# Kernel tuning notes

Measured on AMD Instinct MI355X. Metric: run time of the kernel, lower is better.

## Reference

```python
import jax, jax.numpy as jnp
import numpy as np

N = 50000
E = 1600000
DIM = 128
RC = 5.0
DEPTH = 3


def setup_inputs() -> dict:
    key = jax.random.key(0)
    kv, ke, ks, kd, kw, kb, krs, ksig = jax.random.split(key, 8)
    v = jax.random.normal(kv, (N, DIM), dtype=jnp.float32)
    # edge distances in [0, rc]
    e = jax.random.uniform(ke, (E, 1), dtype=jnp.float32) * RC
    src = jax.random.randint(ks, (E,), 0, N, dtype=jnp.int32)
    dst = jax.random.randint(kd, (E,), 0, N, dtype=jnp.int32)
    # learned params: A = nn.Linear(dim, dim); rs, sigma = torch.rand(1)
    A_w = jax.random.normal(kw, (DIM, DIM), dtype=jnp.float32) / np.sqrt(DIM)
    A_b = jax.random.normal(kb, (DIM,), dtype=jnp.float32) * 0.01
    rs = jax.random.uniform(krs, (1,), dtype=jnp.float32)
    sigma = jax.random.uniform(ksig, (1,), dtype=jnp.float32)
    return {"v": v, "e": e, "src": src, "dst": dst,
            "A_w": A_w, "A_b": A_b, "rs": rs, "sigma": sigma}


def _edge_envelope(r, rs, sigma):
    # exp(-(r-rs)^2/sigma^2) * 0.5 * cos(pi*r/rc) * (r < rc)
    gauss = jnp.exp(-jnp.square(r - rs) / jnp.square(sigma))
    cutoff = 0.5 * jnp.cos(np.pi * r / RC) * (r < RC).astype(r.dtype)
    return gauss * cutoff


def reference(v, e, src, dst, A_w, A_b, rs, sigma):
    f = _edge_envelope(e, rs, sigma)  # [E, 1]
    cur = v
    for _ in range(DEPTH):
        msg = f * cur[src]  # gather src node feats, weight by edge envelope: [E, DIM]
        svf = jax.ops.segment_sum(msg, dst, num_segments=N)  # scatter-sum to dst: [N, DIM]
        cur = jax.nn.relu((svf + v) @ A_w.T + A_b)  # linear + relu, skip from original v
    return cur
```

## Files before the change

kernel.cpp:

```cpp
#include <hip/hip_runtime.h>
#include <math.h>

#define N_NODES 50000
#define N_PAD   50048
#define N_EDGES 1600000
#define DIM     128
#define RCUT    5.0f
#define NGROUP  (N_PAD / 64)
#define NB_PRE  512
#define CH_PRE  (N_EDGES / NB_PRE)
#define NB_CONV 6250
#define NB_WPREP 8
#define NB_SUB  8
#define B_SUB   (NB_PRE / NB_SUB)
#define XPAD    136
#define NTILE   (N_PAD / 16)

typedef __attribute__((ext_vector_type(8))) __bf16 bf16x8;
typedef __attribute__((ext_vector_type(4))) float  f32x4;

__device__ __forceinline__ float bf_lo(unsigned int u) { return __uint_as_float(u << 16); }
__device__ __forceinline__ float bf_hi(unsigned int u) { return __uint_as_float(u & 0xffff0000u); }
__device__ __forceinline__ unsigned short f2bf(float x) {
    unsigned int u = __float_as_uint(x);
    u += 0x7fffu + ((u >> 16) & 1u);
    return (unsigned short)(u >> 16);
}

__global__ __launch_bounds__(256) void preA_kernel(
        const float* __restrict__ v, unsigned short* __restrict__ vb,
        const float* __restrict__ Aw, uint4* __restrict__ wfrag,
        const int* __restrict__ dst, int* __restrict__ partial) {
    int b = blockIdx.x;
    if (b < NB_CONV) {
        int i = b * 256 + threadIdx.x;
        float4 x = ((const float4*)v)[i];
        uint2 o;
        o.x = (unsigned)f2bf(x.x) | ((unsigned)f2bf(x.y) << 16);
        o.y = (unsigned)f2bf(x.z) | ((unsigned)f2bf(x.w) << 16);
        ((uint2*)vb)[i] = o;
    } else if (b < NB_CONV + NB_WPREP) {
        int t = (b - NB_CONV) * 256 + threadIdx.x;
        int lane = t & 63, nt = (t >> 6) & 7, kk = t >> 9;
        int n  = nt * 16 + (lane & 15);
        int k0 = kk * 32 + (lane >> 4) * 8;
        unsigned short h[8];
        #pragma unroll
        for (int i = 0; i < 8; ++i) h[i] = f2bf(Aw[n * DIM + k0 + i]);
        uint4 o;
        o.x = h[0] | ((unsigned)h[1] << 16); o.y = h[2] | ((unsigned)h[3] << 16);
        o.z = h[4] | ((unsigned)h[5] << 16); o.w = h[6] | ((unsigned)h[7] << 16);
        wfrag[t] = o;
    } else {
        __shared__ int h[NGROUP];
        int cb = b - NB_CONV - NB_WPREP, tid = threadIdx.x;
        for (int g = tid; g < NGROUP; g += 256) h[g] = 0;
        __syncthreads();
        int beg = cb * CH_PRE, end = beg + CH_PRE;
        for (int i = beg + tid; i < end; i += 256)
            atomicAdd(&h[dst[i] >> 6], 1);
        __syncthreads();
        for (int g = tid; g < NGROUP; g += 256) partial[cb * NGROUP + g] = h[g];
    }
}

__global__ __launch_bounds__(256) void ktot2_kernel(const int* __restrict__ partial,
                                                    int* __restrict__ partial2) {
    int gb = blockIdx.x & 3, bb = blockIdx.x >> 2;
    int g = gb * 256 + threadIdx.x;
    if (g >= NGROUP) return;
    int s = 0;
    int b0 = bb * B_SUB;
    for (int b = b0; b < b0 + B_SUB; ++b) s += partial[b * NGROUP + g];
    partial2[bb * NGROUP + g] = s;
}

__global__ __launch_bounds__(256) void kscan_kernel(const int* __restrict__ partial2,
                                                    int* __restrict__ goff) {
    __shared__ int part[256];
    int tid = threadIdx.x;
    int i0 = tid * 4;
    int v[4]; int s = 0;
    #pragma unroll
    for (int k = 0; k < 4; ++k) {
        int i = i0 + k; int t = 0;
        if (i < NGROUP) {
            #pragma unroll
            for (int bb = 0; bb < NB_SUB; ++bb) t += partial2[bb * NGROUP + i];
        }
        v[k] = t; s += t;
    }
    part[tid] = s; __syncthreads();
    for (int d = 1; d < 256; d <<= 1) {
        int val = (tid >= d) ? part[tid - d] : 0;
        __syncthreads(); part[tid] += val; __syncthreads();
    }
    int run = (tid == 0) ? 0 : part[tid - 1];
    #pragma unroll
    for (int k = 0; k < 4; ++k) {
        int i = i0 + k;
        if (i < NGROUP) { goff[i] = run; run += v[k]; }
    }
    if (tid == 0) goff[NGROUP] = N_EDGES;
}

__global__ __launch_bounds__(256) void kbase2_kernel(const int* __restrict__ partial,
                                                     const int* __restrict__ partial2,
                                                     const int* __restrict__ goff,
                                                     int* __restrict__ pbase) {
    int gb = blockIdx.x & 3, bb = blockIdx.x >> 2;
    int g = gb * 256 + threadIdx.x;
    if (g >= NGROUP) return;
    int run = goff[g];
    for (int b2 = 0; b2 < bb; ++b2) run += partial2[b2 * NGROUP + g];
    int b0 = bb * B_SUB;
    for (int b = b0; b < b0 + B_SUB; ++b) {
        pbase[b * NGROUP + g] = run;
        run += partial[b * NGROUP + g];
    }
}

__global__ __launch_bounds__(512) void reorder_kernel(
        const float* __restrict__ e,
        const int*   __restrict__ src,
        const int*   __restrict__ dst,
        const float* __restrict__ rs,
        const float* __restrict__ sigma,
        const int*   __restrict__ pbase,
        int2* __restrict__ metaT) {
    __shared__ int base[NGROUP];
    __shared__ int cnt[NGROUP];
    int b = blockIdx.x, tid = threadIdx.x;
    for (int g = tid; g < NGROUP; g += 512) { base[g] = pbase[b * NGROUP + g]; cnt[g] = 0; }
    __syncthreads();
    float rsv = rs[0], sg = sigma[0];
    int beg = b * CH_PRE, end = beg + CH_PRE;
    for (int i = beg + tid; i < end; i += 512) {
        float r  = e[i];
        float d  = r - rsv;
        float gauss = expf(-(d * d) / (sg * sg));
        float cut   = 0.5f * cosf(r * (float)(M_PI / (double)RCUT));
        cut = (r < RCUT) ? cut : 0.0f;
        float fe = gauss * cut;
        int dn = dst[i];
        int g  = dn >> 6;
        int lr = atomicAdd(&cnt[g], 1);
        metaT[base[g] + lr] = make_int2(src[i] * (DIM * 2) | ((dn & 63) << 24),
                                        __float_as_int(fe));
    }
}

#define EDGE2(mx, mf, rr)                                        \
    do {                                                         \
        float ff = __int_as_float(mf);                           \
        a0 = fmaf(ff, bf_lo(rr), a0);                            \
        a1 = fmaf(ff, bf_hi(rr), a1);                            \
    } while (0)

__device__ __forceinline__ void gather_node(
        const int2* __restrict__ meta, const char* basec,
        int beg, int end, float& a0, float& a1) {
    int c = beg;
    if ((c & 1) && c < end) {
        int2 m = meta[c];
        unsigned rr = *(const unsigned*)(basec + (unsigned)m.x);
        EDGE2(m.x, m.y, rr);
        ++c;
    }
    for (; c + 16 <= end; c += 16) {
        int4 m0 = *(const int4*)(meta + c);
        int4 m1 = *(const int4*)(meta + c + 2);
        int4 m2 = *(const int4*)(meta + c + 4);
        int4 m3 = *(const int4*)(meta + c + 6);
        int4 m4 = *(const int4*)(meta + c + 8);
        int4 m5 = *(const int4*)(meta + c + 10);
        int4 m6 = *(const int4*)(meta + c + 12);
        int4 m7 = *(const int4*)(meta + c + 14);
        unsigned r0  = *(const unsigned*)(basec + (unsigned)m0.x);
        unsigned r1  = *(const unsigned*)(basec + (unsigned)m0.z);
        unsigned r2  = *(const unsigned*)(basec + (unsigned)m1.x);
        unsigned r3  = *(const unsigned*)(basec + (unsigned)m1.z);
        unsigned r4  = *(const unsigned*)(basec + (unsigned)m2.x);
        unsigned r5  = *(const unsigned*)(basec + (unsigned)m2.z);
        unsigned r6  = *(const unsigned*)(basec + (unsigned)m3.x);
        unsigned r7  = *(const unsigned*)(basec + (unsigned)m3.z);
        unsigned r8  = *(const unsigned*)(basec + (unsigned)m4.x);
        unsigned r9  = *(const unsigned*)(basec + (unsigned)m4.z);
        unsigned r10 = *(const unsigned*)(basec + (unsigned)m5.x);
        unsigned r11 = *(const unsigned*)(basec + (unsigned)m5.z);
        unsigned r12 = *(const unsigned*)(basec + (unsigned)m6.x);
        unsigned r13 = *(const unsigned*)(basec + (unsigned)m6.z);
        unsigned r14 = *(const unsigned*)(basec + (unsigned)m7.x);
        unsigned r15 = *(const unsigned*)(basec + (unsigned)m7.z);
        EDGE2(m0.x, m0.y, r0);  EDGE2(m0.z, m0.w, r1);
        EDGE2(m1.x, m1.y, r2);  EDGE2(m1.z, m1.w, r3);
        EDGE2(m2.x, m2.y, r4);  EDGE2(m2.z, m2.w, r5);
        EDGE2(m3.x, m3.y, r6);  EDGE2(m3.z, m3.w, r7);
        EDGE2(m4.x, m4.y, r8);  EDGE2(m4.z, m4.w, r9);
        EDGE2(m5.x, m5.y, r10); EDGE2(m5.z, m5.w, r11);
        EDGE2(m6.x, m6.y, r12); EDGE2(m6.z, m6.w, r13);
        EDGE2(m7.x, m7.y, r14); EDGE2(m7.z, m7.w, r15);
    }
    if (c + 8 <= end) {
        int4 m0 = *(const int4*)(meta + c);
        int4 m1 = *(const int4*)(meta + c + 2);
        int4 m2 = *(const int4*)(meta + c + 4);
        int4 m3 = *(const int4*)(meta + c + 6);
        unsigned r0 = *(const unsigned*)(basec + (unsigned)m0.x);
        unsigned r1 = *(const unsigned*)(basec + (unsigned)m0.z);
        unsigned r2 = *(const unsigned*)(basec + (unsigned)m1.x);
        unsigned r3 = *(const unsigned*)(basec + (unsigned)m1.z);
        unsigned r4 = *(const unsigned*)(basec + (unsigned)m2.x);
        unsigned r5 = *(const unsigned*)(basec + (unsigned)m2.z);
        unsigned r6 = *(const unsigned*)(basec + (unsigned)m3.x);
        unsigned r7 = *(const unsigned*)(basec + (unsigned)m3.z);
        EDGE2(m0.x, m0.y, r0); EDGE2(m0.z, m0.w, r1);
        EDGE2(m1.x, m1.y, r2); EDGE2(m1.z, m1.w, r3);
        EDGE2(m2.x, m2.y, r4); EDGE2(m2.z, m2.w, r5);
        EDGE2(m3.x, m3.y, r6); EDGE2(m3.z, m3.w, r7);
        c += 8;
    }
    for (; c < end; ++c) {
        int2 m = meta[c];
        unsigned rr = *(const unsigned*)(basec + (unsigned)m.x);
        EDGE2(m.x, m.y, rr);
    }
}

__global__ __launch_bounds__(512) void layer0_kernel(
        const unsigned short* __restrict__ cur,
        const unsigned short* __restrict__ vb,
        const int2*  __restrict__ metaT,
        const int*   __restrict__ goff,
        int2* __restrict__ meta,
        int*  __restrict__ off,
        const uint4* __restrict__ wfrag,
        const float* __restrict__ bias,
        unsigned short* __restrict__ out_bf) {
    __shared__ unsigned short xlds[64 * XPAD];
    __shared__ int c64[64], b64[65], cu64[64];
    int tid = threadIdx.x;
    int wv  = tid >> 6, lane = tid & 63;
    int g   = blockIdx.x;
    int sbeg = goff[g], send = goff[g + 1];

    if (tid < 64) c64[tid] = 0;
    __syncthreads();
    for (int i = sbeg + tid; i < send; i += 512)
        atomicAdd(&c64[(metaT[i].x >> 24) & 63], 1);
    __syncthreads();
    if (tid == 0) {
        int run = 0;
        #pragma unroll
        for (int t = 0; t < 64; ++t) { b64[t] = run; cu64[t] = run; run += c64[t]; }
        b64[64] = run;
    }
    __syncthreads();
    if (tid < 64) {
        int node = g * 64 + tid;
        if (node <= N_NODES) off[node] = sbeg + b64[tid];
    }
    for (int i = sbeg + tid; i < send; i += 512) {
        int2 m = metaT[i];
        int tag = (m.x >> 24) & 63;
        int lr = atomicAdd(&cu64[tag], 1);
        meta[sbeg + lr] = make_int2(m.x & 0x00FFFFFF, m.y);
    }
    __syncthreads();

    int n0 = g * 64 + wv * 8;
    int myoff = 0;
    if (lane < 9) myoff = sbeg + b64[wv * 8 + lane];
    const char* basec = (const char*)cur + lane * 4;

    #pragma unroll 1
    for (int q = 0; q < 8; ++q) {
        int nl = wv * 8 + q;
        int n  = n0 + q;
        float a0 = 0.f, a1 = 0.f;
        if (n < N_NODES) {
            unsigned vv = *(const unsigned*)((const char*)vb + (size_t)n * (DIM * 2) + lane * 4);
            a0 = bf_lo(vv); a1 = bf_hi(vv);
            int beg = __builtin_amdgcn_readlane(myoff, q);
            int end = __builtin_amdgcn_readlane(myoff, q + 1);
            gather_node(meta, basec, beg, end, a0, a1);
        }
        *(unsigned*)(xlds + nl * XPAD + lane * 2) =
            (unsigned)f2bf(a0) | ((unsigned)f2bf(a1) << 16);
    }
    __syncthreads();

    int quad = lane >> 4, l16 = lane & 15;
    int rb = wv >> 1, nh = wv & 1;
    f32x4 acc[4];
    #pragma unroll
    for (int j = 0; j < 4; ++j) acc[j] = (f32x4){0.f, 0.f, 0.f, 0.f};

    const unsigned short* xp = xlds + (rb * 16 + l16) * XPAD + quad * 8;
    #pragma unroll
    for (int kk = 0; kk < 4; ++kk) {
        bf16x8 af = *(const bf16x8*)(xp + kk * 32);
        #pragma unroll
        for (int j = 0; j < 4; ++j) {
            uint4 w = wfrag[(kk * 8 + nh * 4 + j) * 64 + lane];
            bf16x8 bfr = __builtin_bit_cast(bf16x8, w);
            acc[j] = __builtin_amdgcn_mfma_f32_16x16x32_bf16(af, bfr, acc[j], 0, 0, 0);
        }
    }

    int orow0 = g * 64 + rb * 16 + quad * 4;
    #pragma unroll
    for (int j = 0; j < 4; ++j) {
        int col = (nh * 4 + j) * 16 + l16;
        float b = bias[col];
        #pragma unroll
        for (int r = 0; r < 4; ++r) {
            int orow = orow0 + r;
            if (orow < N_NODES)
                out_bf[(size_t)orow * DIM + col] = f2bf(fmaxf(acc[j][r] + b, 0.f));
        }
    }
}

__global__ __launch_bounds__(128, 8) void layer12_kernel(
        const unsigned short* __restrict__ cur,
        const unsigned short* __restrict__ vb,
        const int2*  __restrict__ meta,
        const int*   __restrict__ off,
        const uint4* __restrict__ wfrag,
        const float* __restrict__ bias,
        unsigned short* __restrict__ out_bf,
        float* __restrict__ out_f,
        int last) {
    __shared__ unsigned short xlds[16 * XPAD];
    int tid = threadIdx.x;
    int wv  = tid >> 6, lane = tid & 63;
    int tile = blockIdx.x;
    int n0  = tile * 16 + wv * 8;

    int offidx = n0 + ((lane < 9) ? lane : 8);
    if (offidx > N_NODES) offidx = N_NODES;
    int myoff = off[offidx];
    const char* basec = (const char*)cur + lane * 4;

    #pragma unroll 1
    for (int q = 0; q < 8; ++q) {
        int nl = wv * 8 + q;
        int n  = n0 + q;
        float a0 = 0.f, a1 = 0.f;
        if (n < N_NODES) {
            unsigned vv = *(const unsigned*)((const char*)vb + (size_t)n * (DIM * 2) + lane * 4);
            a0 = bf_lo(vv); a1 = bf_hi(vv);
            int beg = __builtin_amdgcn_readlane(myoff, q);
            int end = __builtin_amdgcn_readlane(myoff, q + 1);
            gather_node(meta, basec, beg, end, a0, a1);
        }
        *(unsigned*)(xlds + nl * XPAD + lane * 2) =
            (unsigned)f2bf(a0) | ((unsigned)f2bf(a1) << 16);
    }
    __syncthreads();

    int quad = lane >> 4, l16 = lane & 15;
    f32x4 acc[4];
    #pragma unroll
    for (int j = 0; j < 4; ++j) acc[j] = (f32x4){0.f, 0.f, 0.f, 0.f};

    const unsigned short* xp = xlds + l16 * XPAD + quad * 8;
    #pragma unroll
    for (int kk = 0; kk < 4; ++kk) {
        bf16x8 af = *(const bf16x8*)(xp + kk * 32);
        #pragma unroll
        for (int j = 0; j < 4; ++j) {
            uint4 w = wfrag[(kk * 8 + wv * 4 + j) * 64 + lane];
            bf16x8 bfr = __builtin_bit_cast(bf16x8, w);
            acc[j] = __builtin_amdgcn_mfma_f32_16x16x32_bf16(af, bfr, acc[j], 0, 0, 0);
        }
    }

    int orow0 = tile * 16 + quad * 4;
    #pragma unroll
    for (int j = 0; j < 4; ++j) {
        int col = (wv * 4 + j) * 16 + l16;
        float b = bias[col];
        #pragma unroll
        for (int r = 0; r < 4; ++r) {
            int orow = orow0 + r;
            if (orow < N_NODES) {
                float val = fmaxf(acc[j][r] + b, 0.f);
                if (last) out_f[(size_t)orow * DIM + col] = val;
                else      out_bf[(size_t)orow * DIM + col] = f2bf(val);
            }
        }
    }
}

extern "C" void kernel_launch(void* const* d_in, const int* in_sizes, int n_in,
                              void* d_out, int out_size, void* d_ws, size_t ws_size,
                              hipStream_t stream) {
    const float* v     = (const float*)d_in[0];
    const float* e     = (const float*)d_in[1];
    const int*   src   = (const int*)  d_in[2];
    const int*   dst   = (const int*)  d_in[3];
    const float* Aw    = (const float*)d_in[4];
    const float* Ab    = (const float*)d_in[5];
    const float* rs    = (const float*)d_in[6];
    const float* sigma = (const float*)d_in[7];
    float* out = (float*)d_out;

    char* p = (char*)d_ws;
    int2*           meta  = (int2*)p;            p += (size_t)N_EDGES * 8;
    unsigned short* bufV  = (unsigned short*)p;  p += (size_t)N_PAD * DIM * 2;
    unsigned short* bufA  = (unsigned short*)p;  p += (size_t)N_PAD * DIM * 2;
    unsigned short* bufB  = (unsigned short*)p;  p += (size_t)N_PAD * DIM * 2;
    uint4*          wfrag = (uint4*)p;           p += 2048 * 16;
    int*            off   = (int*)p;             p += (size_t)(N_NODES + 1) * 4;
    int*            goff  = (int*)p;             p += (NGROUP + 2) * 4;
    int2* metaT    = (int2*)bufA;
    int*  partial  = (int*)bufB;
    int*  pbase    = partial + NB_PRE * NGROUP;
    int*  partial2 = pbase + NB_PRE * NGROUP;

    preA_kernel<<<NB_CONV + NB_WPREP + NB_PRE, 256, 0, stream>>>(
        v, bufV, Aw, wfrag, dst, partial);
    ktot2_kernel<<<4 * NB_SUB, 256, 0, stream>>>(partial, partial2);
    kscan_kernel<<<1, 256, 0, stream>>>(partial2, goff);
    kbase2_kernel<<<4 * NB_SUB, 256, 0, stream>>>(partial, partial2, goff, pbase);
    reorder_kernel<<<NB_PRE, 512, 0, stream>>>(e, src, dst, rs, sigma, pbase, metaT);

    layer0_kernel<<<NGROUP, 512, 0, stream>>>(
        bufV, bufV, metaT, goff, meta, off, wfrag, Ab, bufB);
    layer12_kernel<<<NTILE, 128, 0, stream>>>(
        bufB, bufV, meta, off, wfrag, Ab, bufA, nullptr, 0);
    layer12_kernel<<<NTILE, 128, 0, stream>>>(
        bufA, bufV, meta, off, wfrag, Ab, nullptr, out, 1);
}
```

Before: 332.7 us.

## Replace multi-kernel partial-count scan with global atomics and per-wave local counters

Drops the per-block partial-count arrays and the two extra reduction/base kernels. Histogram blocks now atomically add group counts into padded global totals, and reorder blocks recount their own chunk and claim base offsets with global atomics after a single scan. In layer0, per-wave counters plus a wavefront shuffle scan replace the single-thread serial prefix, and shared-atomic contention drops. This cuts two launches and a memset-style pass, but adds a memset, a redundant dst read in reorder, and nondeterministic ordering of edges within a group.

Result: slower. 371.1 us (+11.5%).

```diff
diff --git a/kernel.cpp b/kernel.cpp
--- a/kernel.cpp
+++ b/kernel.cpp
@@ -7,14 +7,15 @@
 #define DIM     128
 #define RCUT    5.0f
 #define NGROUP  (N_PAD / 64)
-#define NB_PRE  512
-#define CH_PRE  (N_EDGES / NB_PRE)
 #define NB_CONV 6250
 #define NB_WPREP 8
-#define NB_SUB  8
-#define B_SUB   (NB_PRE / NB_SUB)
+#define NB_HIST 512
+#define CH_HIST (N_EDGES / NB_HIST)
+#define NB_RE   512
+#define CH_RE   (N_EDGES / NB_RE)
 #define XPAD    136
 #define NTILE   (N_PAD / 16)
+#define GPAD    32
 
 typedef __attribute__((ext_vector_type(8))) __bf16 bf16x8;
 typedef __attribute__((ext_vector_type(4))) float  f32x4;
@@ -27,10 +28,10 @@
     return (unsigned short)(u >> 16);
 }
 
-__global__ __launch_bounds__(256) void preA_kernel(
+__global__ __launch_bounds__(256) void pre_kernel(
         const float* __restrict__ v, unsigned short* __restrict__ vb,
         const float* __restrict__ Aw, uint4* __restrict__ wfrag,
-        const int* __restrict__ dst, int* __restrict__ partial) {
+        const int* __restrict__ dst, int* __restrict__ gtotP) {
     int b = blockIdx.x;
     if (b < NB_CONV) {
         int i = b * 256 + threadIdx.x;
@@ -56,39 +57,26 @@
         int cb = b - NB_CONV - NB_WPREP, tid = threadIdx.x;
         for (int g = tid; g < NGROUP; g += 256) h[g] = 0;
         __syncthreads();
-        int beg = cb * CH_PRE, end = beg + CH_PRE;
+        int beg = cb * CH_HIST, end = beg + CH_HIST;
         for (int i = beg + tid; i < end; i += 256)
             atomicAdd(&h[dst[i] >> 6], 1);
         __syncthreads();
-        for (int g = tid; g < NGROUP; g += 256) partial[cb * NGROUP + g] = h[g];
-    }
-}
-
-__global__ __launch_bounds__(256) void ktot2_kernel(const int* __restrict__ partial,
-                                                    int* __restrict__ partial2) {
-    int gb = blockIdx.x & 3, bb = blockIdx.x >> 2;
-    int g = gb * 256 + threadIdx.x;
-    if (g >= NGROUP) return;
-    int s = 0;
-    int b0 = bb * B_SUB;
-    for (int b = b0; b < b0 + B_SUB; ++b) s += partial[b * NGROUP + g];
-    partial2[bb * NGROUP + g] = s;
-}
-
-__global__ __launch_bounds__(256) void kscan_kernel(const int* __restrict__ partial2,
-                                                    int* __restrict__ goff) {
+        for (int g = tid; g < NGROUP; g += 256)
+            if (h[g]) atomicAdd(&gtotP[g * GPAD], h[g]);
+    }
+}
+
+__global__ __launch_bounds__(256) void kscan_kernel(const int* __restrict__ gtotP,
+                                                    int* __restrict__ goff,
+                                                    int* __restrict__ gcurP) {
     __shared__ int part[256];
     int tid = threadIdx.x;
     int i0 = tid * 4;
     int v[4]; int s = 0;
     #pragma unroll
     for (int k = 0; k < 4; ++k) {
-        int i = i0 + k; int t = 0;
-        if (i < NGROUP) {
-            #pragma unroll
-            for (int bb = 0; bb < NB_SUB; ++bb) t += partial2[bb * NGROUP + i];
-        }
-        v[k] = t; s += t;
+        int i = i0 + k;
+        v[k] = (i < NGROUP) ? gtotP[i * GPAD] : 0; s += v[k];
     }
     part[tid] = s; __syncthreads();
     for (int d = 1; d < 256; d <<= 1) {
@@ -99,25 +87,9 @@
     #pragma unroll
     for (int k = 0; k < 4; ++k) {
         int i = i0 + k;
-        if (i < NGROUP) { goff[i] = run; run += v[k]; }
+        if (i < NGROUP) { goff[i] = run; gcurP[i * GPAD] = run; run += v[k]; }
     }
     if (tid == 0) goff[NGROUP] = N_EDGES;
-}
-
-__global__ __launch_bounds__(256) void kbase2_kernel(const int* __restrict__ partial,
-                                                     const int* __restrict__ partial2,
-                                                     const int* __restrict__ goff,
-                                                     int* __restrict__ pbase) {
-    int gb = blockIdx.x & 3, bb = blockIdx.x >> 2;
-    int g = gb * 256 + threadIdx.x;
-    if (g >= NGROUP) return;
-    int run = goff[g];
-    for (int b2 = 0; b2 < bb; ++b2) run += partial2[b2 * NGROUP + g];
-    int b0 = bb * B_SUB;
-    for (int b = b0; b < b0 + B_SUB; ++b) {
-        pbase[b * NGROUP + g] = run;
-        run += partial[b * NGROUP + g];
-    }
 }
 
 __global__ __launch_bounds__(512) void reorder_kernel(
@@ -126,15 +98,24 @@
         const int*   __restrict__ dst,
         const float* __restrict__ rs,
         const float* __restrict__ sigma,
-        const int*   __restrict__ pbase,
+        int*  __restrict__ gcurP,
         int2* __restrict__ metaT) {
     __shared__ int base[NGROUP];
     __shared__ int cnt[NGROUP];
     int b = blockIdx.x, tid = threadIdx.x;
-    for (int g = tid; g < NGROUP; g += 512) { base[g] = pbase[b * NGROUP + g]; cnt[g] = 0; }
+    for (int g = tid; g < NGROUP; g += 512) cnt[g] = 0;
+    __syncthreads();
+    int beg = b * CH_RE, end = beg + CH_RE;
+    for (int i = beg + tid; i < end; i += 512)
+        atomicAdd(&cnt[dst[i] >> 6], 1);
+    __syncthreads();
+    for (int g = tid; g < NGROUP; g += 512) {
+        int c = cnt[g];
+        base[g] = c ? atomicAdd(&gcurP[g * GPAD], c) : 0;
+        cnt[g] = 0;
+    }
     __syncthreads();
     float rsv = rs[0], sg = sigma[0];
-    int beg = b * CH_PRE, end = beg + CH_PRE;
     for (int i = beg + tid; i < end; i += 512) {
         float r  = e[i];
         float d  = r - rsv;
@@ -238,32 +219,43 @@
         const float* __restrict__ bias,
         unsigned short* __restrict__ out_bf) {
     __shared__ unsigned short xlds[64 * XPAD];
-    __shared__ int c64[64], b64[65], cu64[64];
+    __shared__ int cnt8[8][64];
+    __shared__ int wcur[8][64];
+    __shared__ int b64[65];
     int tid = threadIdx.x;
     int wv  = tid >> 6, lane = tid & 63;
     int g   = blockIdx.x;
     int sbeg = goff[g], send = goff[g + 1];
 
-    if (tid < 64) c64[tid] = 0;
+    ((int*)cnt8)[tid] = 0;
     __syncthreads();
     for (int i = sbeg + tid; i < send; i += 512)
-        atomicAdd(&c64[(metaT[i].x >> 24) & 63], 1);
-    __syncthreads();
-    if (tid == 0) {
-        int run = 0;
-        #pragma unroll
-        for (int t = 0; t < 64; ++t) { b64[t] = run; cu64[t] = run; run += c64[t]; }
-        b64[64] = run;
-    }
+        atomicAdd(&cnt8[wv][(metaT[i].x >> 24) & 63], 1);
     __syncthreads();
     if (tid < 64) {
+        int x = 0;
+        #pragma unroll
+        for (int w = 0; w < 8; ++w) x += cnt8[w][tid];
+        int incl = x;
+        #pragma unroll
+        for (int d = 1; d < 64; d <<= 1) {
+            int y = __shfl_up(incl, d, 64);
+            if (tid >= d) incl += y;
+        }
+        int excl = incl - x;
+        b64[tid] = excl;
+        if (tid == 63) b64[64] = incl;
+        int run = excl;
+        #pragma unroll
+        for (int w = 0; w < 8; ++w) { wcur[w][tid] = run; run += cnt8[w][tid]; }
         int node = g * 64 + tid;
-        if (node <= N_NODES) off[node] = sbeg + b64[tid];
-    }
+        if (node <= N_NODES) off[node] = sbeg + excl;
+    }
+    __syncthreads();
     for (int i = sbeg + tid; i < send; i += 512) {
         int2 m = metaT[i];
         int tag = (m.x >> 24) & 63;
-        int lr = atomicAdd(&cu64[tag], 1);
+        int lr = atomicAdd(&wcur[wv][tag], 1);
         meta[sbeg + lr] = make_int2(m.x & 0x00FFFFFF, m.y);
     }
     __syncthreads();
@@ -413,19 +405,17 @@
     unsigned short* bufA  = (unsigned short*)p;  p += (size_t)N_PAD * DIM * 2;
     unsigned short* bufB  = (unsigned short*)p;  p += (size_t)N_PAD * DIM * 2;
     uint4*          wfrag = (uint4*)p;           p += 2048 * 16;
-    int*            off   = (int*)p;             p += (size_t)(N_NODES + 1) * 4;
+    int*            off   = (int*)p;             p += (size_t)(N_NODES + 2) * 4;
     int*            goff  = (int*)p;             p += (NGROUP + 2) * 4;
-    int2* metaT    = (int2*)bufA;
-    int*  partial  = (int*)bufB;
-    int*  pbase    = partial + NB_PRE * NGROUP;
-    int*  partial2 = pbase + NB_PRE * NGROUP;
-
-    preA_kernel<<<NB_CONV + NB_WPREP + NB_PRE, 256, 0, stream>>>(
-        v, bufV, Aw, wfrag, dst, partial);
-    ktot2_kernel<<<4 * NB_SUB, 256, 0, stream>>>(partial, partial2);
-    kscan_kernel<<<1, 256, 0, stream>>>(partial2, goff);
-    kbase2_kernel<<<4 * NB_SUB, 256, 0, stream>>>(partial, partial2, goff, pbase);
-    reorder_kernel<<<NB_PRE, 512, 0, stream>>>(e, src, dst, rs, sigma, pbase, metaT);
+    int*            gtotP = (int*)p;             p += NGROUP * GPAD * 4;
+    int*            gcurP = (int*)p;             p += NGROUP * GPAD * 4;
+    int2* metaT = (int2*)bufA;
+
+    hipMemsetAsync(gtotP, 0, NGROUP * GPAD * 4, stream);
+    pre_kernel<<<NB_CONV + NB_WPREP + NB_HIST, 256, 0, stream>>>(
+        v, bufV, Aw, wfrag, dst, gtotP);
+    kscan_kernel<<<1, 256, 0, stream>>>(gtotP, goff, gcurP);
+    reorder_kernel<<<NB_RE, 512, 0, stream>>>(e, src, dst, rs, sigma, gcurP, metaT);
 
     layer0_kernel<<<NGROUP, 512, 0, stream>>>(
         bufV, bufV, metaT, goff, meta, off, wfrag, Ab, bufB);
```

## Enlarge layer blocks to 64-node groups and coarsen reorder blocks

Applied to the files above, without the earlier changes.

The layer kernel now processes 64 nodes per 512-thread block instead of 16 per 128-thread block. Each wave handles 8 nodes' gathers and then a 16-row by 64-column slice of the MFMA tile, which cuts the block count and amortises weight-fragment loads across more rows. The reorder kernel now runs 128 blocks, each covering four prefix-sum chunks and reading its base offsets from the first chunk of its group. Larger blocks may lower occupancy. Edge order within a group changes, which is only correct if the per-chunk bases are contiguous.

Result: slower. 361.0 us (+8.5%).

```diff
diff --git a/kernel.cpp b/kernel.cpp
--- a/kernel.cpp
+++ b/kernel.cpp
@@ -13,8 +13,9 @@
 #define NB_WPREP 8
 #define NB_SUB  8
 #define B_SUB   (NB_PRE / NB_SUB)
+#define NB_RE   128
+#define CH_RE   (N_EDGES / NB_RE)
 #define XPAD    136
-#define NTILE   (N_PAD / 16)
 
 typedef __attribute__((ext_vector_type(8))) __bf16 bf16x8;
 typedef __attribute__((ext_vector_type(4))) float  f32x4;
@@ -131,10 +132,12 @@
     __shared__ int base[NGROUP];
     __shared__ int cnt[NGROUP];
     int b = blockIdx.x, tid = threadIdx.x;
-    for (int g = tid; g < NGROUP; g += 512) { base[g] = pbase[b * NGROUP + g]; cnt[g] = 0; }
+    for (int g = tid; g < NGROUP; g += 512) {
+        base[g] = pbase[(b * 4) * NGROUP + g]; cnt[g] = 0;
+    }
     __syncthreads();
     float rsv = rs[0], sg = sigma[0];
-    int beg = b * CH_PRE, end = beg + CH_PRE;
+    int beg = b * CH_RE, end = beg + CH_RE;
     for (int i = beg + tid; i < end; i += 512) {
         float r  = e[i];
         float d  = r - rsv;
@@ -322,7 +325,7 @@
     }
 }
 
-__global__ __launch_bounds__(128, 8) void layer12_kernel(
+__global__ __launch_bounds__(512, 6) void layer_kernel(
         const unsigned short* __restrict__ cur,
         const unsigned short* __restrict__ vb,
         const int2*  __restrict__ meta,
@@ -332,11 +335,11 @@
         unsigned short* __restrict__ out_bf,
         float* __restrict__ out_f,
         int last) {
-    __shared__ unsigned short xlds[16 * XPAD];
-    int tid = threadIdx.x;
-    int wv  = tid >> 6, lane = tid & 63;
-    int tile = blockIdx.x;
-    int n0  = tile * 16 + wv * 8;
+    __shared__ unsigned short xlds[64 * XPAD];
+    int tid  = threadIdx.x;
+    int wv   = tid >> 6, lane = tid & 63;
+    int g    = blockIdx.x;
+    int n0   = g * 64 + wv * 8;
 
     int offidx = n0 + ((lane < 9) ? lane : 8);
     if (offidx > N_NODES) offidx = N_NODES;
@@ -361,26 +364,27 @@
     __syncthreads();
 
     int quad = lane >> 4, l16 = lane & 15;
+    int rb = wv >> 1, nh = wv & 1;
     f32x4 acc[4];
     #pragma unroll
     for (int j = 0; j < 4; ++j) acc[j] = (f32x4){0.f, 0.f, 0.f, 0.f};
 
-    const unsigned short* xp = xlds + l16 * XPAD + quad * 8;
+    const unsigned short* xp = xlds + (rb * 16 + l16) * XPAD + quad * 8;
     #pragma unroll
     for (int kk = 0; kk < 4; ++kk) {
         bf16x8 af = *(const bf16x8*)(xp + kk * 32);
         #pragma unroll
         for (int j = 0; j < 4; ++j) {
-            uint4 w = wfrag[(kk * 8 + wv * 4 + j) * 64 + lane];
+            uint4 w = wfrag[(kk * 8 + nh * 4 + j) * 64 + lane];
             bf16x8 bfr = __builtin_bit_cast(bf16x8, w);
             acc[j] = __builtin_amdgcn_mfma_f32_16x16x32_bf16(af, bfr, acc[j], 0, 0, 0);
         }
     }
 
-    int orow0 = tile * 16 + quad * 4;
+    int orow0 = g * 64 + rb * 16 + quad * 4;
     #pragma unroll
     for (int j = 0; j < 4; ++j) {
-        int col = (wv * 4 + j) * 16 + l16;
+        int col = (nh * 4 + j) * 16 + l16;
         float b = bias[col];
         #pragma unroll
         for (int r = 0; r < 4; ++r) {
@@ -413,7 +417,7 @@
     unsigned short* bufA  = (unsigned short*)p;  p += (size_t)N_PAD * DIM * 2;
     unsigned short* bufB  = (unsigned short*)p;  p += (size_t)N_PAD * DIM * 2;
     uint4*          wfrag = (uint4*)p;           p += 2048 * 16;
-    int*            off   = (int*)p;             p += (size_t)(N_NODES + 1) * 4;
+    int*            off   = (int*)p;             p += (size_t)(N_NODES + 2) * 4;
     int*            goff  = (int*)p;             p += (NGROUP + 2) * 4;
     int2* metaT    = (int2*)bufA;
     int*  partial  = (int*)bufB;
@@ -425,12 +429,12 @@
     ktot2_kernel<<<4 * NB_SUB, 256, 0, stream>>>(partial, partial2);
     kscan_kernel<<<1, 256, 0, stream>>>(partial2, goff);
     kbase2_kernel<<<4 * NB_SUB, 256, 0, stream>>>(partial, partial2, goff, pbase);
-    reorder_kernel<<<NB_PRE, 512, 0, stream>>>(e, src, dst, rs, sigma, pbase, metaT);
+    reorder_kernel<<<NB_RE, 512, 0, stream>>>(e, src, dst, rs, sigma, pbase, metaT);
 
     layer0_kernel<<<NGROUP, 512, 0, stream>>>(
         bufV, bufV, metaT, goff, meta, off, wfrag, Ab, bufB);
-    layer12_kernel<<<NTILE, 128, 0, stream>>>(
+    layer_kernel<<<NGROUP, 512, 0, stream>>>(
         bufB, bufV, meta, off, wfrag, Ab, bufA, nullptr, 0);
-    layer12_kernel<<<NTILE, 128, 0, stream>>>(
+    layer_kernel<<<NGROUP, 512, 0, stream>>>(
         bufA, bufV, meta, off, wfrag, Ab, nullptr, out, 1);
 }
```

## Drop base kernel, coarsen reorder blocks, use per-wave local histograms in layer0

Applied to the files above, without the earlier changes.

Removes the kbase2 kernel: ktot2 now writes 4-block partial sums and 64-block totals, and each reorder block computes its own base offsets from goff plus those sums. The reorder pass runs on 128 blocks, each handling four of the histogram chunks. In layer0, per-wave private counters replace the shared 64-bin counters, and the serial single-thread scan becomes a wave shuffle scan, which cuts LDS atomic contention and serialisation. The cost is fewer reorder blocks, so less parallelism for the scatter, plus extra prefix reads at the start of each block.

Measured after the change: 344.5 us. 1.04x slower.

```diff
diff --git a/kernel.cpp b/kernel.cpp
--- a/kernel.cpp
+++ b/kernel.cpp
@@ -11,10 +11,11 @@
 #define CH_PRE  (N_EDGES / NB_PRE)
 #define NB_CONV 6250
 #define NB_WPREP 8
-#define NB_SUB  8
-#define B_SUB   (NB_PRE / NB_SUB)
+#define NB_RE   128
+#define CH_RE   (N_EDGES / NB_RE)
 #define XPAD    136
 #define NTILE   (N_PAD / 16)
+#define BST     65
 
 typedef __attribute__((ext_vector_type(8))) __bf16 bf16x8;
 typedef __attribute__((ext_vector_type(4))) float  f32x4;
@@ -65,17 +66,25 @@
 }
 
 __global__ __launch_bounds__(256) void ktot2_kernel(const int* __restrict__ partial,
-                                                    int* __restrict__ partial2) {
-    int gb = blockIdx.x & 3, bb = blockIdx.x >> 2;
+                                                    int* __restrict__ partial4,
+                                                    int* __restrict__ sum64) {
+    int gb = blockIdx.x & 3, qq = blockIdx.x >> 2;
     int g = gb * 256 + threadIdx.x;
     if (g >= NGROUP) return;
-    int s = 0;
-    int b0 = bb * B_SUB;
-    for (int b = b0; b < b0 + B_SUB; ++b) s += partial[b * NGROUP + g];
-    partial2[bb * NGROUP + g] = s;
-}
-
-__global__ __launch_bounds__(256) void kscan_kernel(const int* __restrict__ partial2,
+    int acc = 0;
+    #pragma unroll 1
+    for (int j = 0; j < 16; ++j) {
+        int s4 = 0;
+        #pragma unroll
+        for (int c = 0; c < 4; ++c)
+            s4 += partial[(qq * 64 + j * 4 + c) * NGROUP + g];
+        partial4[(qq * 16 + j) * NGROUP + g] = s4;
+        acc += s4;
+    }
+    sum64[qq * NGROUP + g] = acc;
+}
+
+__global__ __launch_bounds__(256) void kscan_kernel(const int* __restrict__ sum64,
                                                     int* __restrict__ goff) {
     __shared__ int part[256];
     int tid = threadIdx.x;
@@ -86,7 +95,7 @@
         int i = i0 + k; int t = 0;
         if (i < NGROUP) {
             #pragma unroll
-            for (int bb = 0; bb < NB_SUB; ++bb) t += partial2[bb * NGROUP + i];
+            for (int qq = 0; qq < 8; ++qq) t += sum64[qq * NGROUP + i];
         }
         v[k] = t; s += t;
     }
@@ -102,22 +111,6 @@
         if (i < NGROUP) { goff[i] = run; run += v[k]; }
     }
     if (tid == 0) goff[NGROUP] = N_EDGES;
-}
-
-__global__ __launch_bounds__(256) void kbase2_kernel(const int* __restrict__ partial,
-                                                     const int* __restrict__ partial2,
-                                                     const int* __restrict__ goff,
-                                                     int* __restrict__ pbase) {
-    int gb = blockIdx.x & 3, bb = blockIdx.x >> 2;
-    int g = gb * 256 + threadIdx.x;
-    if (g >= NGROUP) return;
-    int run = goff[g];
-    for (int b2 = 0; b2 < bb; ++b2) run += partial2[b2 * NGROUP + g];
-    int b0 = bb * B_SUB;
-    for (int b = b0; b < b0 + B_SUB; ++b) {
-        pbase[b * NGROUP + g] = run;
-        run += partial[b * NGROUP + g];
-    }
 }
 
 __global__ __launch_bounds__(512) void reorder_kernel(
@@ -126,15 +119,23 @@
         const int*   __restrict__ dst,
         const float* __restrict__ rs,
         const float* __restrict__ sigma,
-        const int*   __restrict__ pbase,
+        const int*   __restrict__ goff,
+        const int*   __restrict__ partial4,
+        const int*   __restrict__ sum64,
         int2* __restrict__ metaT) {
     __shared__ int base[NGROUP];
     __shared__ int cnt[NGROUP];
     int b = blockIdx.x, tid = threadIdx.x;
-    for (int g = tid; g < NGROUP; g += 512) { base[g] = pbase[b * NGROUP + g]; cnt[g] = 0; }
+    int q = b >> 4;
+    for (int g = tid; g < NGROUP; g += 512) {
+        int run = goff[g];
+        for (int qq = 0; qq < q; ++qq) run += sum64[qq * NGROUP + g];
+        for (int j = q * 16; j < b; ++j) run += partial4[j * NGROUP + g];
+        base[g] = run; cnt[g] = 0;
+    }
     __syncthreads();
     float rsv = rs[0], sg = sigma[0];
-    int beg = b * CH_PRE, end = beg + CH_PRE;
+    int beg = b * CH_RE, end = beg + CH_RE;
     for (int i = beg + tid; i < end; i += 512) {
         float r  = e[i];
         float d  = r - rsv;
@@ -238,32 +239,42 @@
         const float* __restrict__ bias,
         unsigned short* __restrict__ out_bf) {
     __shared__ unsigned short xlds[64 * XPAD];
-    __shared__ int c64[64], b64[65], cu64[64];
+    __shared__ int cntW[8 * BST];
+    __shared__ int curW[8 * BST];
+    __shared__ int b64[65];
     int tid = threadIdx.x;
     int wv  = tid >> 6, lane = tid & 63;
     int g   = blockIdx.x;
     int sbeg = goff[g], send = goff[g + 1];
 
-    if (tid < 64) c64[tid] = 0;
+    for (int i = tid; i < 8 * BST; i += 512) cntW[i] = 0;
     __syncthreads();
     for (int i = sbeg + tid; i < send; i += 512)
-        atomicAdd(&c64[(metaT[i].x >> 24) & 63], 1);
-    __syncthreads();
-    if (tid == 0) {
-        int run = 0;
-        #pragma unroll
-        for (int t = 0; t < 64; ++t) { b64[t] = run; cu64[t] = run; run += c64[t]; }
-        b64[64] = run;
-    }
+        atomicAdd(&cntW[wv * BST + ((metaT[i].x >> 24) & 63)], 1);
     __syncthreads();
     if (tid < 64) {
+        int x = 0;
+        #pragma unroll
+        for (int w = 0; w < 8; ++w) x += cntW[w * BST + tid];
+        int incl = x;
+        #pragma unroll
+        for (int d = 1; d < 64; d <<= 1) {
+            int y = __shfl_up(incl, d, 64);
+            if (tid >= d) incl += y;
+        }
+        int excl = incl - x;
+        b64[tid] = excl;
+        if (tid == 63) b64[64] = incl;
+        int run = excl;
+        #pragma unroll
+        for (int w = 0; w < 8; ++w) { curW[w * BST + tid] = run; run += cntW[w * BST + tid]; }
         int node = g * 64 + tid;
-        if (node <= N_NODES) off[node] = sbeg + b64[tid];
-    }
+        if (node <= N_NODES) off[node] = sbeg + excl;
+    }
+    __syncthreads();
     for (int i = sbeg + tid; i < send; i += 512) {
         int2 m = metaT[i];
-        int tag = (m.x >> 24) & 63;
-        int lr = atomicAdd(&cu64[tag], 1);
+        int lr = atomicAdd(&curW[wv * BST + ((m.x >> 24) & 63)], 1);
         meta[sbeg + lr] = make_int2(m.x & 0x00FFFFFF, m.y);
     }
     __syncthreads();
@@ -413,19 +424,19 @@
     unsigned short* bufA  = (unsigned short*)p;  p += (size_t)N_PAD * DIM * 2;
     unsigned short* bufB  = (unsigned short*)p;  p += (size_t)N_PAD * DIM * 2;
     uint4*          wfrag = (uint4*)p;           p += 2048 * 16;
-    int*            off   = (int*)p;             p += (size_t)(N_NODES + 1) * 4;
+    int*            off   = (int*)p;             p += (size_t)(N_NODES + 2) * 4;
     int*            goff  = (int*)p;             p += (NGROUP + 2) * 4;
     int2* metaT    = (int2*)bufA;
     int*  partial  = (int*)bufB;
-    int*  pbase    = partial + NB_PRE * NGROUP;
-    int*  partial2 = pbase + NB_PRE * NGROUP;
+    int*  partial4 = partial + NB_PRE * NGROUP;
+    int*  sum64    = partial4 + 128 * NGROUP;
 
     preA_kernel<<<NB_CONV + NB_WPREP + NB_PRE, 256, 0, stream>>>(
         v, bufV, Aw, wfrag, dst, partial);
-    ktot2_kernel<<<4 * NB_SUB, 256, 0, stream>>>(partial, partial2);
-    kscan_kernel<<<1, 256, 0, stream>>>(partial2, goff);
-    kbase2_kernel<<<4 * NB_SUB, 256, 0, stream>>>(partial, partial2, goff, pbase);
-    reorder_kernel<<<NB_PRE, 512, 0, stream>>>(e, src, dst, rs, sigma, pbase, metaT);
+    ktot2_kernel<<<32, 256, 0, stream>>>(partial, partial4, sum64);
+    kscan_kernel<<<1, 256, 0, stream>>>(sum64, goff);
+    reorder_kernel<<<NB_RE, 512, 0, stream>>>(
+        e, src, dst, rs, sigma, goff, partial4, sum64, metaT);
 
     layer0_kernel<<<NGROUP, 512, 0, stream>>>(
         bufV, bufV, metaT, goff, meta, off, wfrag, Ab, bufB);
```
